# Optimization experiments

Measured on AMD Instinct MI355X. Metric: run time of the kernel, lower is better.

## Reference

```python
import jax, jax.numpy as jnp
import numpy as np

D = 1024
H = 16
DK = D // H


def setup_inputs() -> dict:
    key = jax.random.key(0)
    ks = jax.random.split(key, 10)
    B, S = 2, 2048
    scale = 1.0 / np.sqrt(D)
    inp = {
        "x": jax.random.normal(ks[0], (B, S, D), dtype=jnp.float32),
        "mask": jax.random.randint(ks[1], (B, S), 0, 2, dtype=jnp.int32),
        "wq": jax.random.normal(ks[2], (D, D), dtype=jnp.float32) * scale,
        "bq": jnp.zeros((D,), dtype=jnp.float32),
        "wk": jax.random.normal(ks[3], (D, D), dtype=jnp.float32) * scale,
        "bk": jnp.zeros((D,), dtype=jnp.float32),
        "wv": jax.random.normal(ks[4], (D, D), dtype=jnp.float32) * scale,
        "bv": jnp.zeros((D,), dtype=jnp.float32),
        "wo": jax.random.normal(ks[5], (D, D), dtype=jnp.float32) * scale,
        "bo": jnp.zeros((D,), dtype=jnp.float32),
    }
    return inp


def reference(x, mask, wq, bq, wk, bk, wv, bv, wo, bo):
    B, S, _ = x.shape
    # torch Linear: y = x @ W.T + b
    def proj(w, b):
        return (jnp.einsum("bsd,ed->bse", x, w) + b).reshape(B, S, H, DK).transpose(0, 2, 1, 3)  # (B,H,S,dk)

    q = proj(wq, bq)
    k = proj(wk, bk)
    v = proj(wv, bv)

    scores = jnp.einsum("bhqd,bhkd->bhqk", q, k) / jnp.sqrt(jnp.float32(DK))  # (B,H,S,S)
    # original: mask.unsqueeze(1).unsqueeze(3) -> (B,1,S,1), masks along the QUERY axis
    m = mask[:, None, :, None]  # (B,1,S,1)
    scores = jnp.where(m == 0, jnp.float32(-1e9), scores)
    attn = jax.nn.softmax(scores, axis=-1)
    ctx = jnp.einsum("bhqk,bhkd->bhqd", attn, v)  # (B,H,S,dk)
    concat = ctx.transpose(0, 2, 1, 3).reshape(B, S, D)
    return jnp.einsum("bsd,ed->bse", concat, wo) + bo
```

## Files before the change

kernel.cpp:

```cpp
#include <hip/hip_runtime.h>
#include <hip/hip_bf16.h>

#define SEQ 2048
#define DM  1024

typedef __attribute__((ext_vector_type(8))) _Float16 f16x8;
typedef __attribute__((ext_vector_type(4)))  float   f32x4;

#define EXP2F(x) __builtin_amdgcn_exp2f(x)

__device__ __forceinline__ ushort f2h(float x) {
    union { _Float16 h; ushort u; } c; c.h = (_Float16)x; return c.u;
}

__device__ __forceinline__ void gload16(const void* g, void* l) {
    __builtin_amdgcn_global_load_lds(
        (const __attribute__((address_space(1))) unsigned*)(uintptr_t)g,
        (__attribute__((address_space(3))) unsigned*)(uintptr_t)l, 16, 0, 0);
}

__global__ __launch_bounds__(256)
void cvt_all(const float* __restrict__ x,  const float* __restrict__ wq,
             const float* __restrict__ wk, const float* __restrict__ wv,
             const float* __restrict__ wo,
             ushort* __restrict__ xH, ushort* __restrict__ wH)
{
    const int NX4 = (2 * SEQ * DM) / 4;
    const int NW4 = (DM * DM) / 4;
    const int total = NX4 + 4 * NW4;
    for (int i = blockIdx.x * 256 + threadIdx.x; i < total; i += gridDim.x * 256) {
        float4 v; ushort4* dst;
        if (i < NX4) {
            v = ((const float4*)x)[i];
            dst = (ushort4*)xH + i;
        } else {
            const int j = i - NX4;
            const int wi = j >> 18;
            const int jo = j & (NW4 - 1);
            const float* ws_ = (wi == 0) ? wq : (wi == 1) ? wk : (wi == 2) ? wv : wo;
            v = ((const float4*)ws_)[jo];
            dst = (ushort4*)wH + j;
        }
        ushort4 h;
        h.x = f2h(v.x); h.y = f2h(v.y); h.z = f2h(v.z); h.w = f2h(v.w);
        *dst = h;
    }
}

template<int BM, int BN, int WM, int WN, int MODE>
__global__ __launch_bounds__(WM * WN * 64)
void gemm5(const ushort* __restrict__ A, const ushort* __restrict__ B,
           const float* __restrict__ b0, const float* __restrict__ b1,
           const float* __restrict__ b2,
           ushort* __restrict__ QH, ushort* __restrict__ KH,
           ushort* __restrict__ VH, float* __restrict__ outf, int nmt)
{
    constexpr int NW  = WM * WN;
    constexpr int PR  = BM / WM, PC = BN / WN;
    constexpr int MR  = PR / 16, NR = PC / 16, MH = MR / 2;
    constexpr int APW = (BM / 8) / NW;
    constexpr int BPW = (BN / 8) / NW;
    constexpr int NT  = DM / 64;

    __shared__ ushort A_lds[2][BM * 64];
    __shared__ ushort B_lds[2][BN * 64];

    const int tid = threadIdx.x, w = tid >> 6, lane = tid & 63;
    const int nwg = gridDim.x, q8 = nwg >> 3;
    const int wg  = (blockIdx.x & 7) * q8 + (blockIdx.x >> 3);
    const int m0  = (wg % nmt) * BM, n0 = (wg / nmt) * BN;
    const int wm  = w / WN, wn = w % WN;

    auto stage = [&](int buf, int kt) {
        const int k0 = kt * 64;
#pragma unroll
        for (int j = 0; j < APW; ++j) {
            const int s   = w * APW + j;
            const int row = s * 8 + (lane >> 3);
            const int cl  = (lane & 7) ^ (row & 7);
            gload16(A + (size_t)(m0 + row) * DM + k0 + cl * 8,
                    &A_lds[buf][s * 512]);
        }
#pragma unroll
        for (int j = 0; j < BPW; ++j) {
            const int s   = w * BPW + j;
            const int row = s * 8 + (lane >> 3);
            const int cl  = (lane & 7) ^ (row & 7);
            gload16(B + (size_t)(n0 + row) * DM + k0 + cl * 8,
                    &B_lds[buf][s * 512]);
        }
    };

    f32x4 acc[MR][NR];
#pragma unroll
    for (int i = 0; i < MR; ++i)
#pragma unroll
        for (int j = 0; j < NR; ++j) acc[i][j] = f32x4{0.f, 0.f, 0.f, 0.f};

    stage(0, 0);
    stage(1, 1);

    for (int t = 0; t < NT; ++t) {
        const int buf = t & 1;
        if (t == NT - 1) asm volatile("s_waitcnt vmcnt(0)" ::: "memory");
        else             asm volatile("s_waitcnt vmcnt(8)" ::: "memory");
        __builtin_amdgcn_sched_barrier(0);
        __builtin_amdgcn_s_barrier();

        f16x8 bf_[NR][2];
#pragma unroll
        for (int nf = 0; nf < NR; ++nf) {
            const int r = wn * PC + nf * 16 + (lane & 15);
#pragma unroll
            for (int kb = 0; kb < 2; ++kb) {
                const int c = kb * 4 + (lane >> 4);
                bf_[nf][kb] = *(const f16x8*)&B_lds[buf][r * 64 + ((c ^ (r & 7)) << 3)];
            }
        }
#pragma unroll
        for (int qm = 0; qm < 2; ++qm) {
            f16x8 af_[MH][2];
#pragma unroll
            for (int mf = 0; mf < MH; ++mf) {
                const int r = wm * PR + qm * (PR / 2) + mf * 16 + (lane & 15);
#pragma unroll
                for (int kb = 0; kb < 2; ++kb) {
                    const int c = kb * 4 + (lane >> 4);
                    af_[mf][kb] = *(const f16x8*)&A_lds[buf][r * 64 + ((c ^ (r & 7)) << 3)];
                }
            }
            __builtin_amdgcn_s_setprio(1);
#pragma unroll
            for (int kb = 0; kb < 2; ++kb)
#pragma unroll
                for (int mf = 0; mf < MH; ++mf)
#pragma unroll
                    for (int nf = 0; nf < NR; ++nf)
                        acc[qm * MH + mf][nf] = __builtin_amdgcn_mfma_f32_16x16x32_f16(
                            af_[mf][kb], bf_[nf][kb], acc[qm * MH + mf][nf], 0, 0, 0);
            __builtin_amdgcn_s_setprio(0);
        }
        __builtin_amdgcn_sched_barrier(0);
        __builtin_amdgcn_s_barrier();
        __builtin_amdgcn_sched_barrier(0);
        if (t + 2 < NT) stage(buf, t + 2);
    }

#pragma unroll
    for (int mf = 0; mf < MR; ++mf)
#pragma unroll
        for (int nf = 0; nf < NR; ++nf) {
            const int col  = n0 + wn * PC + nf * 16 + (lane & 15);
            const int row0 = m0 + wm * PR + mf * 16 + ((lane >> 4) << 2);
            f32x4 v = acc[mf][nf];
            if constexpr (MODE == 1) {
                float4 o;
                o.x = v[0] + b0[row0 + 0];
                o.y = v[1] + b0[row0 + 1];
                o.z = v[2] + b0[row0 + 2];
                o.w = v[3] + b0[row0 + 3];
                *(float4*)&outf[(size_t)col * DM + row0] = o;
            } else {
                const int sel = row0 >> 10;
                const int e = row0 & 1023;
                const int b = col >> 11, s = col & 2047;
                const int h = e >> 6, dk = e & 63;
                const float* bp = (sel == 0) ? b0 : (sel == 1) ? b1 : b2;
                const float sc = (sel == 0) ? 0.125f * 1.44269504089f : 1.0f;
                const float v0 = (v[0] + bp[e + 0]) * sc;
                const float v1 = (v[1] + bp[e + 1]) * sc;
                const float v2 = (v[2] + bp[e + 2]) * sc;
                const float v3 = (v[3] + bp[e + 3]) * sc;
                const int bh = b * 16 + h;
                ushort4 hv;
                hv.x = f2h(v0); hv.y = f2h(v1); hv.z = f2h(v2); hv.w = f2h(v3);
                if (sel == 0) {
                    const size_t off = ((size_t)bh * SEQ + s) * 64 + dk;
                    *(ushort4*)&QH[off] = hv;
                } else if (sel == 1) {
                    const size_t off = ((size_t)bh * SEQ + s) * 64 + dk;
                    *(ushort4*)&KH[off] = hv;
                } else {
                    const size_t o0 = ((size_t)bh * 64 + dk) * SEQ + s;
                    VH[o0]           = hv.x;
                    VH[o0 + SEQ]     = hv.y;
                    VH[o0 + 2 * SEQ] = hv.z;
                    VH[o0 + 3 * SEQ] = hv.w;
                }
            }
        }
}

__global__ __launch_bounds__(512, 2)
void attn_k(const ushort* __restrict__ QH, const ushort* __restrict__ KH,
            const ushort* __restrict__ VH, const int* __restrict__ mask,
            ushort* __restrict__ ch)
{
    __shared__ ushort Ks[64 * 64];
    __shared__ ushort Vs[64 * 64];
    __shared__ ushort Ps[8][16 * 64];

    const int t = threadIdx.x, w = t >> 6, lane = t & 63;
    const int wg = (blockIdx.x & 7) * 64 + (blockIdx.x >> 3);
    const int bh = wg >> 4, qt = wg & 15;
    const int b = bh >> 4, h = bh & 15;
    const int q0 = qt * 128 + w * 16;
    const size_t base = (size_t)bh * SEQ * 64;
    const int lq = lane & 15, cb = lane >> 4;

    f16x8 qf[2];
#pragma unroll
    for (int kb = 0; kb < 2; ++kb)
        qf[kb] = *(const f16x8*)&QH[base + (size_t)(q0 + lq) * 64 + kb * 32 + cb * 8];

    const int msk = mask[b * SEQ + q0 + lq];

    float m_run = -1e30f, l_run = 0.f;
    f32x4 acc[4];
#pragma unroll
    for (int df = 0; df < 4; ++df) acc[df] = f32x4{0.f, 0.f, 0.f, 0.f};

    f16x8 sK, sV;
    const int sr = t >> 3, scc = t & 7;
    auto stage_load = [&](int kt) {
        sK = *(const f16x8*)&KH[base + (size_t)(kt * 64 + sr) * 64 + scc * 8];
        sV = *(const f16x8*)&VH[base + (size_t)sr * SEQ + kt * 64 + scc * 8];
    };
    auto stage_write = [&]() {
        const int ph = scc ^ (sr & 7);
        *(f16x8*)&Ks[sr * 64 + ph * 8] = sK;
        *(f16x8*)&Vs[sr * 64 + ph * 8] = sV;
    };

    stage_load(0); stage_write();
    __syncthreads();

    for (int kt = 0; kt < SEQ / 64; ++kt) {
        if (kt < SEQ / 64 - 1) stage_load(kt + 1);

        f32x4 st[4];
#pragma unroll
        for (int mf = 0; mf < 4; ++mf) st[mf] = f32x4{0.f, 0.f, 0.f, 0.f};
        __builtin_amdgcn_s_setprio(1);
#pragma unroll
        for (int mf = 0; mf < 4; ++mf) {
            const int r = mf * 16 + lq;
#pragma unroll
            for (int kb = 0; kb < 2; ++kb) {
                const int p = (kb * 4 + cb) ^ (r & 7);
                f16x8 kf = *(const f16x8*)&Ks[r * 64 + p * 8];
                st[mf] = __builtin_amdgcn_mfma_f32_16x16x32_f16(kf, qf[kb], st[mf], 0, 0, 0);
            }
        }
        __builtin_amdgcn_s_setprio(0);

        {
            if (msk == 0) {
#pragma unroll
                for (int mf = 0; mf < 4; ++mf) st[mf] = f32x4{0.f, 0.f, 0.f, 0.f};
            }
            float mx = -1e30f;
#pragma unroll
            for (int mf = 0; mf < 4; ++mf)
#pragma unroll
                for (int r4 = 0; r4 < 4; ++r4) mx = fmaxf(mx, st[mf][r4]);
            if (!__all(mx - m_run <= 8.0f)) {
                mx = fmaxf(mx, __shfl_xor(mx, 16));
                mx = fmaxf(mx, __shfl_xor(mx, 32));
                const float mnew = fmaxf(m_run, mx);
                const float corr = EXP2F(m_run - mnew);
                m_run = mnew;
                l_run *= corr;
#pragma unroll
                for (int df = 0; df < 4; ++df)
#pragma unroll
                    for (int r4 = 0; r4 < 4; ++r4) acc[df][r4] *= corr;
            }
            float ss = 0.f;
#pragma unroll
            for (int mf = 0; mf < 4; ++mf)
#pragma unroll
                for (int r4 = 0; r4 < 4; ++r4) {
                    const float p = EXP2F(st[mf][r4] - m_run);
                    st[mf][r4] = p; ss += p;
                }
            ss += __shfl_xor(ss, 16);
            ss += __shfl_xor(ss, 32);
            l_run += ss;
        }

#pragma unroll
        for (int mf = 0; mf < 4; ++mf) {
            const int key0 = mf * 16 + (cb << 2);
            ushort4 hv;
            hv.x = f2h(st[mf][0]);
            hv.y = f2h(st[mf][1]);
            hv.z = f2h(st[mf][2]);
            hv.w = f2h(st[mf][3]);
            const int c = key0 >> 3, sub = key0 & 7;
            const int p = c ^ (lq & 7);
            *(ushort4*)&Ps[w][lq * 64 + p * 8 + sub] = hv;
        }

        f16x8 pf[2];
#pragma unroll
        for (int kb = 0; kb < 2; ++kb) {
            const int p = (kb * 4 + cb) ^ (lq & 7);
            pf[kb] = *(const f16x8*)&Ps[w][lq * 64 + p * 8];
        }
        __builtin_amdgcn_s_setprio(1);
#pragma unroll
        for (int df = 0; df < 4; ++df) {
            const int r = df * 16 + lq;
#pragma unroll
            for (int kb = 0; kb < 2; ++kb) {
                const int p = (kb * 4 + cb) ^ (r & 7);
                f16x8 vf = *(const f16x8*)&Vs[r * 64 + p * 8];
                acc[df] = __builtin_amdgcn_mfma_f32_16x16x32_f16(vf, pf[kb], acc[df], 0, 0, 0);
            }
        }
        __builtin_amdgcn_s_setprio(0);

        __syncthreads();
        if (kt < SEQ / 64 - 1) {
            stage_write();
            __syncthreads();
        }
    }

    {
        const float inv = 1.0f / l_run;
        const int s = q0 + lq;
#pragma unroll
        for (int df = 0; df < 4; ++df) {
            const int e0 = h * 64 + df * 16 + (cb << 2);
            ushort4 hv;
            hv.x = f2h(acc[df][0] * inv);
            hv.y = f2h(acc[df][1] * inv);
            hv.z = f2h(acc[df][2] * inv);
            hv.w = f2h(acc[df][3] * inv);
            *(ushort4*)&ch[(size_t)(b * SEQ + s) * DM + e0] = hv;
        }
    }
}

extern "C" void kernel_launch(void* const* d_in, const int* in_sizes, int n_in,
                              void* d_out, int out_size, void* d_ws, size_t ws_size,
                              hipStream_t stream)
{
    const float* x  = (const float*)d_in[0];
    const int* mask = (const int*)d_in[1];
    const float* wq = (const float*)d_in[2];
    const float* bq = (const float*)d_in[3];
    const float* wk = (const float*)d_in[4];
    const float* bk = (const float*)d_in[5];
    const float* wv = (const float*)d_in[6];
    const float* bv = (const float*)d_in[7];
    const float* wo = (const float*)d_in[8];
    const float* bo = (const float*)d_in[9];
    float* out = (float*)d_out;

    const size_t M1 = 1024 * 1024;
    ushort* W = (ushort*)d_ws;
    ushort* xH = W;
    ushort* wH = W + 4 * M1;
    ushort* QH = W + 8 * M1;
    ushort* KH = W + 12 * M1;
    ushort* VH = W + 16 * M1;

    cvt_all<<<2048, 256, 0, stream>>>(x, wq, wk, wv, wo, xH, wH);

    gemm5<384, 128, 4, 2, 0><<<256, 512, 0, stream>>>(
        wH, xH, bq, bk, bv, QH, KH, VH, nullptr, 8);

    attn_k<<<512, 512, 0, stream>>>(QH, KH, VH, mask, xH);

    gemm5<128, 128, 2, 2, 1><<<256, 256, 0, stream>>>(
        wH + 3 * M1, xH, bo, nullptr, nullptr,
        nullptr, nullptr, nullptr, out, 8);
}
```

Measured before the change: 113.8 us.

## Double-buffer K/V shared tiles in attention and pack P conversion

Turns the K/V shared-memory staging in the attention kernel into a two-buffer pipeline. Global loads are issued two tiles ahead and the LDS write for the next tile happens at the top of the loop, which removes one __syncthreads per iteration. It also converts probability pairs to fp16 with the packed round-toward-zero conversion instead of four scalar conversions. The cost is doubled K/V LDS usage, which may hurt the 2-blocks-per-CU occupancy target, and RTZ rounding changes the numerics slightly.

```diff
diff --git a/kernel.cpp b/kernel.cpp
--- a/kernel.cpp
+++ b/kernel.cpp
@@ -11,6 +11,12 @@
 
 __device__ __forceinline__ ushort f2h(float x) {
     union { _Float16 h; ushort u; } c; c.h = (_Float16)x; return c.u;
+}
+__device__ __forceinline__ unsigned pk2h(float a, float b) {
+    typedef __fp16 fp16v2 __attribute__((ext_vector_type(2)));
+    union { fp16v2 h; unsigned u; } c;
+    c.h = __builtin_amdgcn_cvt_pkrtz(a, b);
+    return c.u;
 }
 
 __device__ __forceinline__ void gload16(const void* g, void* l) {
@@ -196,8 +202,8 @@
             const ushort* __restrict__ VH, const int* __restrict__ mask,
             ushort* __restrict__ ch)
 {
-    __shared__ ushort Ks[64 * 64];
-    __shared__ ushort Vs[64 * 64];
+    __shared__ ushort Ks[2][64 * 64];
+    __shared__ ushort Vs[2][64 * 64];
     __shared__ ushort Ps[8][16 * 64];
 
     const int t = threadIdx.x, w = t >> 6, lane = t & 63;
@@ -222,21 +228,24 @@
 
     f16x8 sK, sV;
     const int sr = t >> 3, scc = t & 7;
+    const int ph = scc ^ (sr & 7);
     auto stage_load = [&](int kt) {
         sK = *(const f16x8*)&KH[base + (size_t)(kt * 64 + sr) * 64 + scc * 8];
         sV = *(const f16x8*)&VH[base + (size_t)sr * SEQ + kt * 64 + scc * 8];
     };
-    auto stage_write = [&]() {
-        const int ph = scc ^ (sr & 7);
-        *(f16x8*)&Ks[sr * 64 + ph * 8] = sK;
-        *(f16x8*)&Vs[sr * 64 + ph * 8] = sV;
+    auto stage_write = [&](int buf) {
+        *(f16x8*)&Ks[buf][sr * 64 + ph * 8] = sK;
+        *(f16x8*)&Vs[buf][sr * 64 + ph * 8] = sV;
     };
 
-    stage_load(0); stage_write();
+    stage_load(0); stage_write(0);
+    stage_load(1);
     __syncthreads();
 
     for (int kt = 0; kt < SEQ / 64; ++kt) {
-        if (kt < SEQ / 64 - 1) stage_load(kt + 1);
+        const int buf = kt & 1;
+        if (kt + 1 < SEQ / 64) stage_write(buf ^ 1);
+        if (kt + 2 < SEQ / 64) stage_load(kt + 2);
 
         f32x4 st[4];
 #pragma unroll
@@ -248,7 +257,7 @@
 #pragma unroll
             for (int kb = 0; kb < 2; ++kb) {
                 const int p = (kb * 4 + cb) ^ (r & 7);
-                f16x8 kf = *(const f16x8*)&Ks[r * 64 + p * 8];
+                f16x8 kf = *(const f16x8*)&Ks[buf][r * 64 + p * 8];
                 st[mf] = __builtin_amdgcn_mfma_f32_16x16x32_f16(kf, qf[kb], st[mf], 0, 0, 0);
             }
         }
@@ -292,14 +301,12 @@
 #pragma unroll
         for (int mf = 0; mf < 4; ++mf) {
             const int key0 = mf * 16 + (cb << 2);
-            ushort4 hv;
-            hv.x = f2h(st[mf][0]);
-            hv.y = f2h(st[mf][1]);
-            hv.z = f2h(st[mf][2]);
-            hv.w = f2h(st[mf][3]);
+            uint2 pw;
+            pw.x = pk2h(st[mf][0], st[mf][1]);
+            pw.y = pk2h(st[mf][2], st[mf][3]);
             const int c = key0 >> 3, sub = key0 & 7;
             const int p = c ^ (lq & 7);
-            *(ushort4*)&Ps[w][lq * 64 + p * 8 + sub] = hv;
+            *(uint2*)&Ps[w][lq * 64 + p * 8 + sub] = pw;
         }
 
         f16x8 pf[2];
@@ -315,17 +322,13 @@
 #pragma unroll
             for (int kb = 0; kb < 2; ++kb) {
                 const int p = (kb * 4 + cb) ^ (r & 7);
-                f16x8 vf = *(const f16x8*)&Vs[r * 64 + p * 8];
+                f16x8 vf = *(const f16x8*)&Vs[buf][r * 64 + p * 8];
                 acc[df] = __builtin_amdgcn_mfma_f32_16x16x32_f16(vf, pf[kb], acc[df], 0, 0, 0);
             }
         }
         __builtin_amdgcn_s_setprio(0);
 
         __syncthreads();
-        if (kt < SEQ / 64 - 1) {
-            stage_write();
-            __syncthreads();
-        }
     }
 
     {
```

Result: no change. 111.6 us (-1.9%).
